# Optimization experiments

Measured on AMD Instinct MI355X. Metric: run time of the kernel, lower is better.

The kernel has to match this reference:

```python
import jax, jax.numpy as jnp
import numpy as np

N_NODES = 50000
N_EDGES = 800000
D = 128          # node/edge feature dim
H = 128          # MLP hidden dim
T_EDGE = 3       # number of edge types
T_NODE = 2       # number of node types


def setup_inputs() -> dict:
    key = jax.random.key(0)
    ks = jax.random.split(key, 14)
    s = 0.05  # weight init scale
    return {
        "nf": jax.random.normal(ks[0], (N_NODES, D), jnp.float32),
        "ef": jax.random.normal(ks[1], (N_EDGES, D), jnp.float32),
        "src": jax.random.randint(ks[2], (N_EDGES,), 0, N_NODES, jnp.int32),
        "dst": jax.random.randint(ks[3], (N_EDGES,), 0, N_NODES, jnp.int32),
        "etype": jax.random.randint(ks[4], (N_EDGES,), 0, T_EDGE, jnp.int32),
        "ntype": jax.random.randint(ks[5], (N_NODES,), 0, T_NODE, jnp.int32),
        # per-edge-type MLP: Linear(3D->H), ReLU, Linear(H->D)
        "We_h": jax.random.normal(ks[6], (T_EDGE, 3 * D, H), jnp.float32) * s,
        "be_h": jnp.zeros((T_EDGE, H), jnp.float32),
        "We_o": jax.random.normal(ks[7], (T_EDGE, H, D), jnp.float32) * s,
        "be_o": jnp.zeros((T_EDGE, D), jnp.float32),
        # per-node-type MLP: Linear(2D->H), ReLU, Linear(H->D)
        "Wn_h": jax.random.normal(ks[8], (T_NODE, 2 * D, H), jnp.float32) * s,
        "bn_h": jnp.zeros((T_NODE, H), jnp.float32),
        "Wn_o": jax.random.normal(ks[9], (T_NODE, H, D), jnp.float32) * s,
        "bn_o": jnp.zeros((T_NODE, D), jnp.float32),
    }


def _typed_mlp(x, tvec, Wh, bh, Wo, bo):
    """Per-type 2-layer MLP dispatch, then the source's gather-back.

    The torch code builds type_pos_list (stable concat of per-type index lists,
    i.e. a stable argsort of tvec) and then indexes the concatenated per-type
    outputs with that same permutation (`updated[type_perm]`, a gather rather
    than an inverse-permutation scatter). We reproduce that exactly:
    out_final[j] = out_correct[perm[perm[j]]].
    """
    T = Wh.shape[0]
    out = jnp.zeros((x.shape[0], Wo.shape[-1]), x.dtype)
    for k in range(T):  # small fixed number of types
        y = jax.nn.relu(x @ Wh[k] + bh[k]) @ Wo[k] + bo[k]
        out = jnp.where((tvec == k)[:, None], y, out)
    perm = jnp.argsort(tvec)  # jax argsort is stable
    return out[perm[perm]]


def reference(nf, ef, src, dst, etype, ntype,
              We_h, be_h, We_o, be_o, Wn_h, bn_h, Wn_o, bn_o):
    # edge update: cat([ef, src_nf, dst_nf]) -> per-type MLP
    em_in = jnp.concatenate([ef, nf[src], nf[dst]], axis=-1)  # [E, 3D]
    new_ef = _typed_mlp(em_in, etype, We_h, be_h, We_o, be_o)  # [E, D]
    # message passing: copy_e('h') messages, sum reduce into dst nodes
    agg_m = jax.ops.segment_sum(new_ef, dst, num_segments=nf.shape[0])  # [N, D]
    # node update: cat([agg_m, nf]) -> per-type MLP
    nm_in = jnp.concatenate([agg_m, nf], axis=-1)  # [N, 2D]
    new_nf = _typed_mlp(nm_in, ntype, Wn_h, bn_h, Wn_o, bn_o)  # [N, D]
    return new_nf, new_ef
```

## Files before the change

### kernel.cpp

```cpp
#include <hip/hip_runtime.h>

typedef __bf16 bf16_t;
typedef bf16_t bf16x8_t __attribute__((ext_vector_type(8)));
typedef float  f32x4_t  __attribute__((ext_vector_type(4)));

#define RCHUNK 4096

__global__ void pack_w_kernel(const float* __restrict__ W, bf16_t* __restrict__ out,
                              int T, int Ksrc, int k0, int KB)
{
  int total = T * KB * 8 * 512;
  for (int idx = blockIdx.x * blockDim.x + threadIdx.x; idx < total;
       idx += gridDim.x * blockDim.x) {
    int j  = idx & 7;
    int l  = (idx >> 3) & 63;
    int nb = (idx >> 9) & 7;
    int r  = idx >> 12;
    int kb = r % KB;
    int t  = r / KB;
    int k = k0 + kb * 32 + ((l >> 4) << 3) + j;
    int n = nb * 16 + (l & 15);
    out[idx] = (bf16_t)W[((size_t)t * Ksrc + k) * 128 + n];
  }
}

template <int T>
__global__ void count_types_kernel(const int* __restrict__ tv, int n,
                                   int* __restrict__ blkcnt)
{
  __shared__ int cnt[T];
  int tid = threadIdx.x, b = blockIdx.x;
  if (tid < T) cnt[tid] = 0;
  __syncthreads();
  int lo = b * RCHUNK, hi = min(n, lo + RCHUNK);
  int loc[T];
#pragma unroll
  for (int t = 0; t < T; ++t) loc[t] = 0;
  for (int i = lo + tid; i < hi; i += 256) {
    int tq = tv[i];
#pragma unroll
    for (int t = 0; t < T; ++t) loc[t] += (tq == t);
  }
#pragma unroll
  for (int t = 0; t < T; ++t)
    if (loc[t]) atomicAdd(&cnt[t], loc[t]);
  __syncthreads();
  if (tid < T) blkcnt[b * T + tid] = cnt[tid];
}

template <int T>
__global__ void scan_blocks_kernel(const int* __restrict__ blkcnt, int nblocks,
                                   int* __restrict__ blkbase)
{
  __shared__ int sh[256];
  __shared__ int tot[T];
  int tid = threadIdx.x;
  int myc[T], excl[T];
#pragma unroll
  for (int t = 0; t < T; ++t) myc[t] = (tid < nblocks) ? blkcnt[tid * T + t] : 0;
#pragma unroll
  for (int t = 0; t < T; ++t) {
    sh[tid] = myc[t];
    __syncthreads();
    for (int off = 1; off < 256; off <<= 1) {
      int v = (tid >= off) ? sh[tid - off] : 0;
      __syncthreads();
      sh[tid] += v;
      __syncthreads();
    }
    excl[t] = sh[tid] - myc[t];
    if (tid == 255) tot[t] = sh[255];
    __syncthreads();
  }
  if (tid < nblocks) {
    int run = 0;
#pragma unroll
    for (int t = 0; t < T; ++t) {
      blkbase[tid * T + t] = run + excl[t];
      run += tot[t];
    }
  }
}

template <int T>
__global__ void write_ranks_kernel(const int* __restrict__ tv, int n,
                                   const int* __restrict__ blkbase,
                                   int* __restrict__ rank, int* __restrict__ perm)
{
  __shared__ int sh[256];
  int tid = threadIdx.x, b = blockIdx.x;
  int lo = b * RCHUNK + tid * 16;
  int tvq[16];
  int myc[T];
#pragma unroll
  for (int t = 0; t < T; ++t) myc[t] = 0;
#pragma unroll
  for (int q = 0; q < 16; ++q) {
    int i = lo + q;
    int tq = (i < n) ? tv[i] : -1;
    tvq[q] = tq;
#pragma unroll
    for (int t = 0; t < T; ++t) myc[t] += (tq == t);
  }
  int mybase[T];
#pragma unroll
  for (int t = 0; t < T; ++t) {
    sh[tid] = myc[t];
    __syncthreads();
    for (int off = 1; off < 256; off <<= 1) {
      int v = (tid >= off) ? sh[tid - off] : 0;
      __syncthreads();
      sh[tid] += v;
      __syncthreads();
    }
    mybase[t] = blkbase[b * T + t] + sh[tid] - myc[t];
    __syncthreads();
  }
#pragma unroll
  for (int q = 0; q < 16; ++q) {
    int tq = tvq[q];
    if (tq < 0) continue;
    int r = 0;
#pragma unroll
    for (int t = 0; t < T; ++t)
      if (tq == t) { r = mybase[t]; mybase[t] = r + 1; }
    rank[lo + q] = r;
    perm[r] = lo + q;
  }
}

__global__ void hist_dst_kernel(const int* __restrict__ dst, int E,
                                int* __restrict__ hist)
{
  int i = blockIdx.x * blockDim.x + threadIdx.x;
  if (i < E) atomicAdd(&hist[dst[i]], 1);
}

__global__ __launch_bounds__(1024) void scan_offsets_kernel(
    const int* __restrict__ hist, int n, int* __restrict__ offsets,
    int* __restrict__ cursor)
{
  __shared__ int sh[1024];
  int tid = threadIdx.x;
  int per = (n + 1023) >> 10;
  int lo = tid * per;
  int s = 0;
  for (int q = 0; q < per; ++q) {
    int i = lo + q;
    if (i < n) s += hist[i];
  }
  sh[tid] = s;
  __syncthreads();
  for (int off = 1; off < 1024; off <<= 1) {
    int v = (tid >= off) ? sh[tid - off] : 0;
    __syncthreads();
    sh[tid] += v;
    __syncthreads();
  }
  int run = sh[tid] - s;
  for (int q = 0; q < per; ++q) {
    int i = lo + q;
    if (i < n) {
      offsets[i] = run;
      cursor[i] = run;
      run += hist[i];
    }
  }
  if (tid == 1023) offsets[n] = sh[1023];
}

__global__ void scatter_dst_kernel(const int* __restrict__ dst, int E,
                                   int* __restrict__ cursor,
                                   int* __restrict__ edge_by_dst)
{
  int i = blockIdx.x * blockDim.x + threadIdx.x;
  if (i < E) {
    int pos = atomicAdd(&cursor[dst[i]], 1);
    edge_by_dst[pos] = i;
  }
}

__global__ __launch_bounds__(256) void aggregate_kernel(
    const float* __restrict__ ef_new, const int* __restrict__ edge_by_dst,
    const int* __restrict__ offsets, float* __restrict__ agg, int Nn)
{
  int gwid = (blockIdx.x * 256 + threadIdx.x) >> 6;
  int l = threadIdx.x & 63;
  int nw = (gridDim.x * 256) >> 6;
  for (int n = gwid; n < Nn; n += nw) {
    int lo = offsets[n], hi = offsets[n + 1];
    float sx = 0.f, sy = 0.f;
    int q = lo;
    for (; q + 1 < hi; q += 2) {
      int e0 = edge_by_dst[q], e1 = edge_by_dst[q + 1];
      float2 v0 = *(const float2*)(ef_new + (size_t)e0 * 128 + l * 2);
      float2 v1 = *(const float2*)(ef_new + (size_t)e1 * 128 + l * 2);
      sx += v0.x + v1.x;
      sy += v0.y + v1.y;
    }
    if (q < hi) {
      int e0 = edge_by_dst[q];
      float2 v0 = *(const float2*)(ef_new + (size_t)e0 * 128 + l * 2);
      sx += v0.x;
      sy += v0.y;
    }
    float2 o;
    o.x = sx; o.y = sy;
    *(float2*)(agg + (size_t)n * 128 + l * 2) = o;
  }
}

__global__ __launch_bounds__(256) void precompute_p_kernel(
    const float* __restrict__ nf,
    const bf16_t* __restrict__ pW1s, const bf16_t* __restrict__ pW1d,
    const bf16_t* __restrict__ pWn1b,
    bf16_t* __restrict__ Ps, bf16_t* __restrict__ Pd, bf16_t* __restrict__ Pn,
    int Nn)
{
  __shared__ char Wsm[32768];
  const int which = blockIdx.x & 7, tile = blockIdx.x >> 3;
  const bf16_t* pB; bf16_t* po;
  if (which < 3)      { pB = pW1s + which * 16384;        po = Ps + (size_t)which * Nn * 128; }
  else if (which < 6) { pB = pW1d + (which - 3) * 16384;  po = Pd + (size_t)(which - 3) * Nn * 128; }
  else                { pB = pWn1b + (which - 6) * 16384; po = Pn + (size_t)(which - 6) * Nn * 128; }

  const int tid = threadIdx.x, l = tid & 63, w = tid >> 6;
  const int rb = (w >> 1) * 32, cb = (w & 1) * 64, l15 = l & 15;
  const int koff = (l >> 4) << 3;

  {
    const uint4* g = (const uint4*)pB;
    uint4* d = (uint4*)Wsm;
#pragma unroll
    for (int q = 0; q < 8; ++q) d[q * 256 + tid] = g[q * 256 + tid];
  }

  const int base = tile * 64;
  const int r0 = base + rb + l15, r1 = r0 + 16;
  const float* q0 = nf + (size_t)min(r0, Nn - 1) * 128 + koff;
  const float* q1 = nf + (size_t)min(r1, Nn - 1) * 128 + koff;
  f32x4_t areg[2][4][2];
#pragma unroll
  for (int kb = 0; kb < 4; ++kb) {
    areg[0][kb][0] = ((const f32x4_t*)(q0 + kb * 32))[0];
    areg[0][kb][1] = ((const f32x4_t*)(q0 + kb * 32))[1];
    areg[1][kb][0] = ((const f32x4_t*)(q1 + kb * 32))[0];
    areg[1][kb][1] = ((const f32x4_t*)(q1 + kb * 32))[1];
  }
  __syncthreads();

  f32x4_t acc[2][4];
#pragma unroll
  for (int m = 0; m < 2; ++m)
#pragma unroll
    for (int n = 0; n < 4; ++n) acc[m][n] = (f32x4_t){0.f, 0.f, 0.f, 0.f};

#pragma unroll
  for (int kb = 0; kb < 4; ++kb) {
    bf16x8_t bfr[4];
#pragma unroll
    for (int n = 0; n < 4; ++n)
      bfr[n] = *(const bf16x8_t*)(Wsm + ((kb * 8 + (cb >> 4) + n) * 64 + l) * 16);
    bf16x8_t a0, a1;
#pragma unroll
    for (int z = 0; z < 4; ++z) {
      a0[z] = (bf16_t)areg[0][kb][0][z]; a0[4 + z] = (bf16_t)areg[0][kb][1][z];
      a1[z] = (bf16_t)areg[1][kb][0][z]; a1[4 + z] = (bf16_t)areg[1][kb][1][z];
    }
#pragma unroll
    for (int n = 0; n < 4; ++n) {
      acc[0][n] = __builtin_amdgcn_mfma_f32_16x16x32_bf16(a0, bfr[n], acc[0][n], 0, 0, 0);
      acc[1][n] = __builtin_amdgcn_mfma_f32_16x16x32_bf16(a1, bfr[n], acc[1][n], 0, 0, 0);
    }
  }

#pragma unroll
  for (int n = 0; n < 4; ++n) {
    int col = cb + 16 * n + l15;
#pragma unroll
    for (int m = 0; m < 2; ++m)
#pragma unroll
      for (int jj = 0; jj < 4; ++jj) {
        int row = rb + 16 * m + ((l >> 4) << 2) + jj;
        int node = base + row;
        if (node < Nn) po[(size_t)node * 128 + col] = (bf16_t)acc[m][n][jj];
      }
  }
}

template <int T, bool EDGE>
__global__ __launch_bounds__(256, 2) void mlp4_kernel(
    const float* __restrict__ feat,
    const int* __restrict__ src, const int* __restrict__ dst,
    const int* __restrict__ perm, const int* __restrict__ rank,
    const int* __restrict__ tbase,
    const bf16_t* __restrict__ pW1, const float* __restrict__ b1,
    const bf16_t* __restrict__ pW2, const float* __restrict__ b2,
    const bf16_t* __restrict__ P1, const bf16_t* __restrict__ P2, int pnodes,
    float* __restrict__ out, int Ntot)
{
  __shared__ char Wsm[32768];
  __shared__ char Psm[16384];
  __shared__ char Hsm[16384];
  __shared__ int sm_e[64], sm_j[64], sm_s0[64], sm_s1[64];

  const int tid = threadIdx.x;
  const int l = tid & 63, w = tid >> 6;
  const int rb = (w >> 1) * 32, cb = (w & 1) * 64;
  const int l15 = l & 15;
  const int koff = (l >> 4) << 3;

  const int s0 = tbase[0];
  const int s1 = (T > 1) ? tbase[1] : Ntot;
  const int s2 = (T > 2) ? tbase[2] : Ntot;
  const int e0t = (T > 1) ? s1 : Ntot;
  const int e1t = (T > 2) ? s2 : Ntot;
  const int c0 = (e0t - s0 + 63) >> 6;
  const int c1 = (T > 1) ? ((e1t - s1 + 63) >> 6) : 0;
  const int c2 = (T > 2) ? ((Ntot - s2 + 63) >> 6) : 0;
  const int cum1 = c0, cum2 = c0 + c1, total = cum2 + c2;

  const int tpb = (total + gridDim.x - 1) / gridDim.x;
  const int pt0 = blockIdx.x * tpb;
  const int pt1 = min(total, pt0 + tpb);

  int cur_t = -1;
  bf16x8_t w2r[16];
  float bh[4], bo[4];

  for (int pt = pt0; pt < pt1; ++pt) {
    const int t = (pt < cum1) ? 0 : ((pt < cum2) ? 1 : 2);
    const int tstart = (t == 0) ? s0 : ((t == 1) ? s1 : s2);
    const int tend = (t == 0) ? e0t : ((t == 1) ? e1t : Ntot);
    const int i = pt - ((t == 0) ? 0 : ((t == 1) ? cum1 : cum2));
    const int pbase = tstart + (i << 6);

    __syncthreads();
    if (tid < 64) {
      int pos = pbase + tid;
      if (pos < tend) {
        int e = perm[pos];
        sm_e[tid] = e;
        sm_j[tid] = rank[pos];
        if (EDGE) { sm_s0[tid] = src[e]; sm_s1[tid] = dst[e]; }
      } else {
        sm_e[tid] = 0; sm_j[tid] = -1;
        if (EDGE) { sm_s0[tid] = 0; sm_s1[tid] = 0; }
      }
    }
    __syncthreads();

    const int ar0 = rb + l15, ar1 = ar0 + 16;
    const float* q0 = feat + (size_t)sm_e[ar0] * 128 + koff;
    const float* q1 = feat + (size_t)sm_e[ar1] * 128 + koff;
    f32x4_t areg[2][4][2];
#pragma unroll
    for (int kb = 0; kb < 4; ++kb) {
      areg[0][kb][0] = ((const f32x4_t*)(q0 + kb * 32))[0];
      areg[0][kb][1] = ((const f32x4_t*)(q0 + kb * 32))[1];
      areg[1][kb][0] = ((const f32x4_t*)(q1 + kb * 32))[0];
      areg[1][kb][1] = ((const f32x4_t*)(q1 + kb * 32))[1];
    }

#pragma unroll
    for (int q = 0; q < 4; ++q) {
      int idx = tid * 4 + q;
      int row = idx >> 4, c8 = idx & 15;
      bf16x8_t s;
      if (EDGE) {
        bf16x8_t u = ((const bf16x8_t*)(P1 + ((size_t)t * pnodes + sm_s0[row]) * 128))[c8];
        bf16x8_t v = ((const bf16x8_t*)(P2 + ((size_t)t * pnodes + sm_s1[row]) * 128))[c8];
#pragma unroll
        for (int z = 0; z < 8; ++z) s[z] = (bf16_t)((float)u[z] + (float)v[z]);
      } else {
        s = ((const bf16x8_t*)(P1 + ((size_t)t * pnodes + sm_e[row]) * 128))[c8];
      }
      *(bf16x8_t*)(Psm + row * 256 + ((c8 ^ (row & 15)) << 4)) = s;
    }

    if (t != cur_t) {
      __syncthreads();
      {
        const uint4* g = (const uint4*)(pW1 + (size_t)t * 16384);
        uint4* d = (uint4*)Wsm;
#pragma unroll
        for (int q = 0; q < 8; ++q) d[q * 256 + tid] = g[q * 256 + tid];
      }
      {
        const bf16x8_t* g2 = (const bf16x8_t*)pW2;
#pragma unroll
        for (int kb = 0; kb < 4; ++kb)
#pragma unroll
          for (int n = 0; n < 4; ++n)
            w2r[kb * 4 + n] = g2[(size_t)((t * 4 + kb) * 8 + (cb >> 4) + n) * 64 + l];
      }
#pragma unroll
      for (int n = 0; n < 4; ++n) {
        bh[n] = b1[t * 128 + cb + 16 * n + l15];
        bo[n] = b2[t * 128 + cb + 16 * n + l15];
      }
      cur_t = t;
      __syncthreads();
    }

    f32x4_t acc[2][4];
#pragma unroll
    for (int m = 0; m < 2; ++m)
#pragma unroll
      for (int n = 0; n < 4; ++n) acc[m][n] = (f32x4_t){0.f, 0.f, 0.f, 0.f};

#pragma unroll
    for (int kb = 0; kb < 4; ++kb) {
      bf16x8_t bfr[4];
#pragma unroll
      for (int n = 0; n < 4; ++n)
        bfr[n] = *(const bf16x8_t*)(Wsm + ((kb * 8 + (cb >> 4) + n) * 64 + l) * 16);
      bf16x8_t a0, a1;
#pragma unroll
      for (int z = 0; z < 4; ++z) {
        a0[z] = (bf16_t)areg[0][kb][0][z]; a0[4 + z] = (bf16_t)areg[0][kb][1][z];
        a1[z] = (bf16_t)areg[1][kb][0][z]; a1[4 + z] = (bf16_t)areg[1][kb][1][z];
      }
#pragma unroll
      for (int n = 0; n < 4; ++n) {
        acc[0][n] = __builtin_amdgcn_mfma_f32_16x16x32_bf16(a0, bfr[n], acc[0][n], 0, 0, 0);
        acc[1][n] = __builtin_amdgcn_mfma_f32_16x16x32_bf16(a1, bfr[n], acc[1][n], 0, 0, 0);
      }
    }

    __syncthreads();
#pragma unroll
    for (int n = 0; n < 4; ++n) {
      int col = cb + 16 * n + l15;
      int byte = col * 2;
#pragma unroll
      for (int m = 0; m < 2; ++m)
#pragma unroll
        for (int jj = 0; jj < 4; ++jj) {
          int row = rb + 16 * m + ((l >> 4) << 2) + jj;
          float pv = (float)*(const bf16_t*)(
              Psm + row * 256 + ((byte & 15) | ((((byte >> 4) ^ (row & 15)) & 15) << 4)));
          float v = acc[m][n][jj] + pv + bh[n];
          v = v > 0.f ? v : 0.f;
          *(bf16_t*)(Hsm + row * 256 + (byte ^ ((row & 7) << 4))) = (bf16_t)v;
        }
    }
    __syncthreads();

    f32x4_t acc2[2][4];
#pragma unroll
    for (int m = 0; m < 2; ++m)
#pragma unroll
      for (int n = 0; n < 4; ++n) acc2[m][n] = (f32x4_t){0.f, 0.f, 0.f, 0.f};

#pragma unroll
    for (int kb = 0; kb < 4; ++kb) {
      int kbyte = kb * 64 + ((l >> 4) << 4);
      int row0 = rb + l15, row1 = row0 + 16;
      bf16x8_t h0 = *(const bf16x8_t*)(Hsm + row0 * 256 + (kbyte ^ ((row0 & 7) << 4)));
      bf16x8_t h1 = *(const bf16x8_t*)(Hsm + row1 * 256 + (kbyte ^ ((row1 & 7) << 4)));
#pragma unroll
      for (int n = 0; n < 4; ++n) {
        acc2[0][n] = __builtin_amdgcn_mfma_f32_16x16x32_bf16(h0, w2r[kb * 4 + n], acc2[0][n], 0, 0, 0);
        acc2[1][n] = __builtin_amdgcn_mfma_f32_16x16x32_bf16(h1, w2r[kb * 4 + n], acc2[1][n], 0, 0, 0);
      }
    }

#pragma unroll
    for (int n = 0; n < 4; ++n) {
      int col = cb + 16 * n + l15;
#pragma unroll
      for (int m = 0; m < 2; ++m)
#pragma unroll
        for (int jj = 0; jj < 4; ++jj) {
          int row = rb + 16 * m + ((l >> 4) << 2) + jj;
          int j = sm_j[row];
          if (j >= 0) out[(size_t)j * 128 + col] = acc2[m][n][jj] + bo[n];
        }
    }
  }
}

extern "C" void kernel_launch(void* const* d_in, const int* in_sizes, int n_in,
                              void* d_out, int out_size, void* d_ws, size_t ws_size,
                              hipStream_t stream)
{
  const float* nf    = (const float*)d_in[0];
  const float* ef    = (const float*)d_in[1];
  const int*   src   = (const int*)d_in[2];
  const int*   dst   = (const int*)d_in[3];
  const int*   etype = (const int*)d_in[4];
  const int*   ntype = (const int*)d_in[5];
  const float* Weh   = (const float*)d_in[6];
  const float* beh   = (const float*)d_in[7];
  const float* Weo   = (const float*)d_in[8];
  const float* beo   = (const float*)d_in[9];
  const float* Wnh   = (const float*)d_in[10];
  const float* bnh   = (const float*)d_in[11];
  const float* Wno   = (const float*)d_in[12];
  const float* bno   = (const float*)d_in[13];

  const int E = in_sizes[2];
  const int N = in_sizes[5];
  const int TE = 3, TN = 2;

  char* ws = (char*)d_ws;
  size_t off = 0;
  auto alloc = [&](size_t bytes) -> char* {
    char* p = ws + off;
    off = (off + bytes + 511) & ~(size_t)511;
    return p;
  };
  bf16_t* pW1e  = (bf16_t*)alloc((size_t)TE * 16384 * 2);
  bf16_t* pW1s  = (bf16_t*)alloc((size_t)TE * 16384 * 2);
  bf16_t* pW1d  = (bf16_t*)alloc((size_t)TE * 16384 * 2);
  bf16_t* pWe2  = (bf16_t*)alloc((size_t)TE * 16384 * 2);
  bf16_t* pWn1a = (bf16_t*)alloc((size_t)TN * 16384 * 2);
  bf16_t* pWn1b = (bf16_t*)alloc((size_t)TN * 16384 * 2);
  bf16_t* pWn2  = (bf16_t*)alloc((size_t)TN * 16384 * 2);
  bf16_t* Ps = (bf16_t*)alloc((size_t)TE * N * 128 * 2);
  bf16_t* Pd = (bf16_t*)alloc((size_t)TE * N * 128 * 2);
  bf16_t* Pn = (bf16_t*)alloc((size_t)TN * N * 128 * 2);
  int* rank_e = (int*)alloc((size_t)E * 4);
  int* perm_e = (int*)alloc((size_t)E * 4);
  int* rank_n = (int*)alloc((size_t)N * 4);
  int* perm_n = (int*)alloc((size_t)N * 4);
  const int NBE = (E + RCHUNK - 1) / RCHUNK;
  const int NBN = (N + RCHUNK - 1) / RCHUNK;
  int* blkcnt_e  = (int*)alloc((size_t)NBE * TE * 4);
  int* blkbase_e = (int*)alloc((size_t)NBE * TE * 4);
  int* blkcnt_n  = (int*)alloc((size_t)NBN * TN * 4);
  int* blkbase_n = (int*)alloc((size_t)NBN * TN * 4);
  float* agg = (float*)alloc((size_t)N * 128 * 4);
  int* dsthist     = (int*)alloc((size_t)N * 4);
  int* dstoffs     = (int*)alloc((size_t)(N + 1) * 4);
  int* dstcursor   = (int*)alloc((size_t)N * 4);
  int* edge_by_dst = (int*)alloc((size_t)E * 4);
  (void)ws_size; (void)n_in; (void)out_size;

  pack_w_kernel<<<192, 256, 0, stream>>>(Weh, pW1e, TE, 384, 0, 4);
  pack_w_kernel<<<192, 256, 0, stream>>>(Weh, pW1s, TE, 384, 128, 4);
  pack_w_kernel<<<192, 256, 0, stream>>>(Weh, pW1d, TE, 384, 256, 4);
  pack_w_kernel<<<192, 256, 0, stream>>>(Weo, pWe2, TE, 128, 0, 4);
  pack_w_kernel<<<128, 256, 0, stream>>>(Wnh, pWn1a, TN, 256, 0, 4);
  pack_w_kernel<<<128, 256, 0, stream>>>(Wnh, pWn1b, TN, 256, 128, 4);
  pack_w_kernel<<<128, 256, 0, stream>>>(Wno, pWn2, TN, 128, 0, 4);

  const int ptiles = (N + 63) / 64;
  precompute_p_kernel<<<ptiles * 8, 256, 0, stream>>>(
      nf, pW1s, pW1d, pWn1b, Ps, Pd, Pn, N);

  count_types_kernel<3><<<NBE, 256, 0, stream>>>(etype, E, blkcnt_e);
  scan_blocks_kernel<3><<<1, 256, 0, stream>>>(blkcnt_e, NBE, blkbase_e);
  write_ranks_kernel<3><<<NBE, 256, 0, stream>>>(etype, E, blkbase_e, rank_e, perm_e);

  count_types_kernel<2><<<NBN, 256, 0, stream>>>(ntype, N, blkcnt_n);
  scan_blocks_kernel<2><<<1, 256, 0, stream>>>(blkcnt_n, NBN, blkbase_n);
  write_ranks_kernel<2><<<NBN, 256, 0, stream>>>(ntype, N, blkbase_n, rank_n, perm_n);

  hipMemsetAsync(dsthist, 0, (size_t)N * 4, stream);
  hist_dst_kernel<<<(E + 255) / 256, 256, 0, stream>>>(dst, E, dsthist);
  scan_offsets_kernel<<<1, 1024, 0, stream>>>(dsthist, N, dstoffs, dstcursor);
  scatter_dst_kernel<<<(E + 255) / 256, 256, 0, stream>>>(dst, E, dstcursor, edge_by_dst);

  float* out_nf = (float*)d_out;
  float* out_ef = (float*)d_out + (size_t)N * 128;

  mlp4_kernel<3, true><<<512, 256, 0, stream>>>(
      ef, src, dst, perm_e, rank_e, blkbase_e,
      pW1e, beh, pWe2, beo, Ps, Pd, N, out_ef, E);

  aggregate_kernel<<<3200, 256, 0, stream>>>(out_ef, edge_by_dst, dstoffs, agg, N);

  mlp4_kernel<2, false><<<512, 256, 0, stream>>>(
      agg, nullptr, nullptr, perm_n, rank_n, blkbase_n,
      pWn1a, bnh, pWn2, bno, Pn, nullptr, N, out_nf, N);
}
```

Baseline: 840.2 us.

## Software-pipeline MLP gathers and aggregate from dst-sorted bf16 slot buffer

The MLP kernel now prefetches the next tile's feature rows and projected P rows while the current tile computes. Per-row metadata comes from precomputed int4 arrays shuffled across lanes, replacing the LDS staging that needed extra barriers. The edge MLP also writes a bf16 copy of each output row into a dst-sorted slot buffer, so aggregation becomes a contiguous streaming read with no indirect fp32 gathers. The precompute kernel uses a persistent grid that loops over tiles. In exchange this adds two metadata kernels, an extra bf16 write stream of the edge outputs, and bf16 rounding in the aggregated sums, which loses some precision.

```diff
diff --git a/kernel.cpp b/kernel.cpp
--- a/kernel.cpp
+++ b/kernel.cpp
@@ -1,10 +1,12 @@
 #include <hip/hip_runtime.h>
 
 typedef __bf16 bf16_t;
+typedef bf16_t bf16x2_t __attribute__((ext_vector_type(2)));
 typedef bf16_t bf16x8_t __attribute__((ext_vector_type(8)));
 typedef float  f32x4_t  __attribute__((ext_vector_type(4)));
 
 #define RCHUNK 4096
+#define MFMA16(a, b, c) __builtin_amdgcn_mfma_f32_16x16x32_bf16((a), (b), (c), 0, 0, 0)
 
 __global__ void pack_w_kernel(const float* __restrict__ W, bf16_t* __restrict__ out,
                               int T, int Ksrc, int k0, int KB)
@@ -171,41 +173,66 @@
 
 __global__ void scatter_dst_kernel(const int* __restrict__ dst, int E,
                                    int* __restrict__ cursor,
-                                   int* __restrict__ edge_by_dst)
+                                   int* __restrict__ dstpos)
+{
+  int i = blockIdx.x * blockDim.x + threadIdx.x;
+  if (i < E) dstpos[i] = atomicAdd(&cursor[dst[i]], 1);
+}
+
+__global__ void gather_meta_edge_kernel(const int* __restrict__ perm,
+                                        const int* __restrict__ rank,
+                                        const int* __restrict__ src,
+                                        const int* __restrict__ dst,
+                                        const int* __restrict__ dstpos,
+                                        int4* __restrict__ meta4,
+                                        int* __restrict__ slotv, int E)
 {
   int i = blockIdx.x * blockDim.x + threadIdx.x;
   if (i < E) {
-    int pos = atomicAdd(&cursor[dst[i]], 1);
-    edge_by_dst[pos] = i;
-  }
-}
-
-__global__ __launch_bounds__(256) void aggregate_kernel(
-    const float* __restrict__ ef_new, const int* __restrict__ edge_by_dst,
-    const int* __restrict__ offsets, float* __restrict__ agg, int Nn)
-{
-  int gwid = (blockIdx.x * 256 + threadIdx.x) >> 6;
+    int e = perm[i], j = rank[i];
+    int4 m;
+    m.x = e; m.y = src[e]; m.z = dst[e]; m.w = j;
+    meta4[i] = m;
+    slotv[i] = dstpos[j];
+  }
+}
+
+__global__ void gather_meta_node_kernel(const int* __restrict__ perm,
+                                        const int* __restrict__ rank,
+                                        int4* __restrict__ meta4, int N)
+{
+  int i = blockIdx.x * blockDim.x + threadIdx.x;
+  if (i < N) {
+    int e = perm[i];
+    int4 m;
+    m.x = e; m.y = e; m.z = e; m.w = rank[i];
+    meta4[i] = m;
+  }
+}
+
+__global__ __launch_bounds__(256) void aggregate_slots_kernel(
+    const bf16_t* __restrict__ slot_buf, const int* __restrict__ offsets,
+    float* __restrict__ agg, int Nn)
+{
+  int gw = (blockIdx.x * 256 + threadIdx.x) >> 6;
   int l = threadIdx.x & 63;
   int nw = (gridDim.x * 256) >> 6;
-  for (int n = gwid; n < Nn; n += nw) {
+  for (int n = gw; n < Nn; n += nw) {
     int lo = offsets[n], hi = offsets[n + 1];
     float sx = 0.f, sy = 0.f;
     int q = lo;
     for (; q + 1 < hi; q += 2) {
-      int e0 = edge_by_dst[q], e1 = edge_by_dst[q + 1];
-      float2 v0 = *(const float2*)(ef_new + (size_t)e0 * 128 + l * 2);
-      float2 v1 = *(const float2*)(ef_new + (size_t)e1 * 128 + l * 2);
-      sx += v0.x + v1.x;
-      sy += v0.y + v1.y;
+      bf16x2_t v0 = *(const bf16x2_t*)(slot_buf + (size_t)q * 128 + l * 2);
+      bf16x2_t v1 = *(const bf16x2_t*)(slot_buf + (size_t)(q + 1) * 128 + l * 2);
+      sx += (float)v0[0] + (float)v1[0];
+      sy += (float)v0[1] + (float)v1[1];
     }
     if (q < hi) {
-      int e0 = edge_by_dst[q];
-      float2 v0 = *(const float2*)(ef_new + (size_t)e0 * 128 + l * 2);
-      sx += v0.x;
-      sy += v0.y;
-    }
-    float2 o;
-    o.x = sx; o.y = sy;
+      bf16x2_t v0 = *(const bf16x2_t*)(slot_buf + (size_t)q * 128 + l * 2);
+      sx += (float)v0[0];
+      sy += (float)v0[1];
+    }
+    float2 o; o.x = sx; o.y = sy;
     *(float2*)(agg + (size_t)n * 128 + l * 2) = o;
   }
 }
@@ -215,10 +242,11 @@
     const bf16_t* __restrict__ pW1s, const bf16_t* __restrict__ pW1d,
     const bf16_t* __restrict__ pWn1b,
     bf16_t* __restrict__ Ps, bf16_t* __restrict__ Pd, bf16_t* __restrict__ Pn,
-    int Nn)
+    int Nn, int nseg)
 {
   __shared__ char Wsm[32768];
-  const int which = blockIdx.x & 7, tile = blockIdx.x >> 3;
+  const int which = blockIdx.x & 7;
+  const int seg = blockIdx.x >> 3;
   const bf16_t* pB; bf16_t* po;
   if (which < 3)      { pB = pW1s + which * 16384;        po = Ps + (size_t)which * Nn * 128; }
   else if (which < 6) { pB = pW1d + (which - 3) * 16384;  po = Pd + (size_t)(which - 3) * Nn * 128; }
@@ -234,75 +262,73 @@
 #pragma unroll
     for (int q = 0; q < 8; ++q) d[q * 256 + tid] = g[q * 256 + tid];
   }
-
-  const int base = tile * 64;
-  const int r0 = base + rb + l15, r1 = r0 + 16;
-  const float* q0 = nf + (size_t)min(r0, Nn - 1) * 128 + koff;
-  const float* q1 = nf + (size_t)min(r1, Nn - 1) * 128 + koff;
-  f32x4_t areg[2][4][2];
-#pragma unroll
-  for (int kb = 0; kb < 4; ++kb) {
-    areg[0][kb][0] = ((const f32x4_t*)(q0 + kb * 32))[0];
-    areg[0][kb][1] = ((const f32x4_t*)(q0 + kb * 32))[1];
-    areg[1][kb][0] = ((const f32x4_t*)(q1 + kb * 32))[0];
-    areg[1][kb][1] = ((const f32x4_t*)(q1 + kb * 32))[1];
-  }
   __syncthreads();
 
-  f32x4_t acc[2][4];
-#pragma unroll
-  for (int m = 0; m < 2; ++m)
-#pragma unroll
-    for (int n = 0; n < 4; ++n) acc[m][n] = (f32x4_t){0.f, 0.f, 0.f, 0.f};
-
-#pragma unroll
-  for (int kb = 0; kb < 4; ++kb) {
-    bf16x8_t bfr[4];
-#pragma unroll
-    for (int n = 0; n < 4; ++n)
-      bfr[n] = *(const bf16x8_t*)(Wsm + ((kb * 8 + (cb >> 4) + n) * 64 + l) * 16);
-    bf16x8_t a0, a1;
-#pragma unroll
-    for (int z = 0; z < 4; ++z) {
-      a0[z] = (bf16_t)areg[0][kb][0][z]; a0[4 + z] = (bf16_t)areg[0][kb][1][z];
-      a1[z] = (bf16_t)areg[1][kb][0][z]; a1[4 + z] = (bf16_t)areg[1][kb][1][z];
+  const int ntiles = (Nn + 63) >> 6;
+  for (int tile = seg; tile < ntiles; tile += nseg) {
+    const int base = tile * 64;
+    const int r0 = min(base + rb + l15, Nn - 1);
+    const int r1 = min(base + rb + l15 + 16, Nn - 1);
+    const float* q0 = nf + (size_t)r0 * 128 + koff;
+    const float* q1 = nf + (size_t)r1 * 128 + koff;
+    f32x4_t areg[16];
+#pragma unroll
+    for (int kb = 0; kb < 4; ++kb) {
+      areg[kb * 2]     = ((const f32x4_t*)(q0 + kb * 32))[0];
+      areg[kb * 2 + 1] = ((const f32x4_t*)(q0 + kb * 32))[1];
+      areg[8 + kb * 2]     = ((const f32x4_t*)(q1 + kb * 32))[0];
+      areg[8 + kb * 2 + 1] = ((const f32x4_t*)(q1 + kb * 32))[1];
+    }
+    f32x4_t acc[2][4];
+#pragma unroll
+    for (int m = 0; m < 2; ++m)
+#pragma unroll
+      for (int n = 0; n < 4; ++n) acc[m][n] = (f32x4_t){0.f, 0.f, 0.f, 0.f};
+#pragma unroll
+    for (int kb = 0; kb < 4; ++kb) {
+      bf16x8_t bfr[4];
+#pragma unroll
+      for (int n = 0; n < 4; ++n)
+        bfr[n] = *(const bf16x8_t*)(Wsm + ((kb * 8 + (cb >> 4) + n) * 64 + l) * 16);
+      bf16x8_t a0, a1;
+#pragma unroll
+      for (int z = 0; z < 4; ++z) {
+        a0[z] = (bf16_t)areg[kb * 2][z];     a0[4 + z] = (bf16_t)areg[kb * 2 + 1][z];
+        a1[z] = (bf16_t)areg[8 + kb * 2][z]; a1[4 + z] = (bf16_t)areg[8 + kb * 2 + 1][z];
+      }
+#pragma unroll
+      for (int n = 0; n < 4; ++n) {
+        acc[0][n] = MFMA16(a0, bfr[n], acc[0][n]);
+        acc[1][n] = MFMA16(a1, bfr[n], acc[1][n]);
+      }
     }
 #pragma unroll
     for (int n = 0; n < 4; ++n) {
-      acc[0][n] = __builtin_amdgcn_mfma_f32_16x16x32_bf16(a0, bfr[n], acc[0][n], 0, 0, 0);
-      acc[1][n] = __builtin_amdgcn_mfma_f32_16x16x32_bf16(a1, bfr[n], acc[1][n], 0, 0, 0);
-    }
-  }
-
-#pragma unroll
-  for (int n = 0; n < 4; ++n) {
-    int col = cb + 16 * n + l15;
-#pragma unroll
-    for (int m = 0; m < 2; ++m)
-#pragma unroll
-      for (int jj = 0; jj < 4; ++jj) {
-        int row = rb + 16 * m + ((l >> 4) << 2) + jj;
-        int node = base + row;
-        if (node < Nn) po[(size_t)node * 128 + col] = (bf16_t)acc[m][n][jj];
-      }
+      int col = cb + 16 * n + l15;
+#pragma unroll
+      for (int m = 0; m < 2; ++m)
+#pragma unroll
+        for (int jj = 0; jj < 4; ++jj) {
+          int row = rb + 16 * m + ((l >> 4) << 2) + jj;
+          int node = base + row;
+          if (node < Nn) po[(size_t)node * 128 + col] = (bf16_t)acc[m][n][jj];
+        }
+    }
   }
 }
 
 template <int T, bool EDGE>
-__global__ __launch_bounds__(256, 2) void mlp4_kernel(
+__global__ __launch_bounds__(256, 2) void mlp5_kernel(
     const float* __restrict__ feat,
-    const int* __restrict__ src, const int* __restrict__ dst,
-    const int* __restrict__ perm, const int* __restrict__ rank,
+    const int4* __restrict__ meta4, const int* __restrict__ slotv,
     const int* __restrict__ tbase,
     const bf16_t* __restrict__ pW1, const float* __restrict__ b1,
     const bf16_t* __restrict__ pW2, const float* __restrict__ b2,
     const bf16_t* __restrict__ P1, const bf16_t* __restrict__ P2, int pnodes,
-    float* __restrict__ out, int Ntot)
+    float* __restrict__ out, bf16_t* __restrict__ slot_out, int Ntot)
 {
   __shared__ char Wsm[32768];
-  __shared__ char Psm[16384];
   __shared__ char Hsm[16384];
-  __shared__ int sm_e[64], sm_j[64], sm_s0[64], sm_s1[64];
 
   const int tid = threadIdx.x;
   const int l = tid & 63, w = tid >> 6;
@@ -323,62 +349,78 @@
   const int tpb = (total + gridDim.x - 1) / gridDim.x;
   const int pt0 = blockIdx.x * tpb;
   const int pt1 = min(total, pt0 + tpb);
-
-  int cur_t = -1;
+  if (pt0 >= pt1) return;
+
+  auto tinfo_t = [&](int pt) -> int {
+    return (pt < cum1) ? 0 : ((pt < cum2) ? 1 : 2);
+  };
+  auto tinfo_base = [&](int pt) -> int {
+    return (pt < cum1) ? s0 + (pt << 6)
+         : (pt < cum2) ? s1 + ((pt - cum1) << 6)
+                       : s2 + ((pt - cum2) << 6);
+  };
+  auto tinfo_end = [&](int pt) -> int {
+    return (pt < cum1) ? e0t : ((pt < cum2) ? e1t : Ntot);
+  };
+  auto load_meta = [&](int pt, int4& m, int& sl) {
+    int pos = tinfo_base(pt) + l;
+    int p = min(pos, Ntot - 1);
+    m = meta4[p];
+    if (EDGE) sl = slotv[p];
+    if (pos >= tinfo_end(pt)) m.w = -1;
+  };
+
+  const int prow = (w << 4) + (l >> 2);
+  const int pcb  = (l & 3) << 2;
+
+  int4 m_cur, m_nxt;
+  int sl_cur = 0, sl_nxt = 0;
+  f32x4_t Af[16];
+  bf16x8_t uP[4], vP[4], ps[4];
   bf16x8_t w2r[16];
   float bh[4], bo[4];
+  int t_cur = -1;
+
+  load_meta(pt0, m_cur, sl_cur);
+  {
+    int e0 = __shfl(m_cur.x, rb + l15);
+    int e1 = __shfl(m_cur.x, rb + l15 + 16);
+    const float* q0 = feat + (size_t)e0 * 128 + koff;
+    const float* q1 = feat + (size_t)e1 * 128 + koff;
+#pragma unroll
+    for (int kb = 0; kb < 4; ++kb) {
+      Af[kb * 2]     = ((const f32x4_t*)(q0 + kb * 32))[0];
+      Af[kb * 2 + 1] = ((const f32x4_t*)(q0 + kb * 32))[1];
+      Af[8 + kb * 2]     = ((const f32x4_t*)(q1 + kb * 32))[0];
+      Af[8 + kb * 2 + 1] = ((const f32x4_t*)(q1 + kb * 32))[1];
+    }
+    int t0 = tinfo_t(pt0);
+    int a = __shfl(EDGE ? m_cur.y : m_cur.x, prow);
+    const bf16x8_t* pu = (const bf16x8_t*)(P1 + ((size_t)t0 * pnodes + a) * 128);
+#pragma unroll
+    for (int q = 0; q < 4; ++q) uP[q] = pu[pcb + q];
+    if (EDGE) {
+      int bi = __shfl(m_cur.z, prow);
+      const bf16x8_t* pv = (const bf16x8_t*)(P2 + ((size_t)t0 * pnodes + bi) * 128);
+#pragma unroll
+      for (int q = 0; q < 4; ++q) vP[q] = pv[pcb + q];
+    }
+  }
+  if (EDGE) {
+#pragma unroll
+    for (int q = 0; q < 4; ++q)
+#pragma unroll
+      for (int z = 0; z < 8; ++z)
+        ps[q][z] = (bf16_t)((float)uP[q][z] + (float)vP[q][z]);
+  } else {
+#pragma unroll
+    for (int q = 0; q < 4; ++q) ps[q] = uP[q];
+  }
+  load_meta(min(pt0 + 1, pt1 - 1), m_nxt, sl_nxt);
 
   for (int pt = pt0; pt < pt1; ++pt) {
-    const int t = (pt < cum1) ? 0 : ((pt < cum2) ? 1 : 2);
-    const int tstart = (t == 0) ? s0 : ((t == 1) ? s1 : s2);
-    const int tend = (t == 0) ? e0t : ((t == 1) ? e1t : Ntot);
-    const int i = pt - ((t == 0) ? 0 : ((t == 1) ? cum1 : cum2));
-    const int pbase = tstart + (i << 6);
-
-    __syncthreads();
-    if (tid < 64) {
-      int pos = pbase + tid;
-      if (pos < tend) {
-        int e = perm[pos];
-        sm_e[tid] = e;
-        sm_j[tid] = rank[pos];
-        if (EDGE) { sm_s0[tid] = src[e]; sm_s1[tid] = dst[e]; }
-      } else {
-        sm_e[tid] = 0; sm_j[tid] = -1;
-        if (EDGE) { sm_s0[tid] = 0; sm_s1[tid] = 0; }
-      }
-    }
-    __syncthreads();
-
-    const int ar0 = rb + l15, ar1 = ar0 + 16;
-    const float* q0 = feat + (size_t)sm_e[ar0] * 128 + koff;
-    const float* q1 = feat + (size_t)sm_e[ar1] * 128 + koff;
-    f32x4_t areg[2][4][2];
-#pragma unroll
-    for (int kb = 0; kb < 4; ++kb) {
-      areg[0][kb][0] = ((const f32x4_t*)(q0 + kb * 32))[0];
-      areg[0][kb][1] = ((const f32x4_t*)(q0 + kb * 32))[1];
-      areg[1][kb][0] = ((const f32x4_t*)(q1 + kb * 32))[0];
-      areg[1][kb][1] = ((const f32x4_t*)(q1 + kb * 32))[1];
-    }
-
-#pragma unroll
-    for (int q = 0; q < 4; ++q) {
-      int idx = tid * 4 + q;
-      int row = idx >> 4, c8 = idx & 15;
-      bf16x8_t s;
-      if (EDGE) {
-        bf16x8_t u = ((const bf16x8_t*)(P1 + ((size_t)t * pnodes + sm_s0[row]) * 128))[c8];
-        bf16x8_t v = ((const bf16x8_t*)(P2 + ((size_t)t * pnodes + sm_s1[row]) * 128))[c8];
-#pragma unroll
-        for (int z = 0; z < 8; ++z) s[z] = (bf16_t)((float)u[z] + (float)v[z]);
-      } else {
-        s = ((const bf16x8_t*)(P1 + ((size_t)t * pnodes + sm_e[row]) * 128))[c8];
-      }
-      *(bf16x8_t*)(Psm + row * 256 + ((c8 ^ (row & 15)) << 4)) = s;
-    }
-
-    if (t != cur_t) {
+    const int t = tinfo_t(pt);
+    if (t != t_cur) {
       __syncthreads();
       {
         const uint4* g = (const uint4*)(pW1 + (size_t)t * 16384);
@@ -399,7 +441,7 @@
         bh[n] = b1[t * 128 + cb + 16 * n + l15];
         bo[n] = b2[t * 128 + cb + 16 * n + l15];
       }
-      cur_t = t;
+      t_cur = t;
       __syncthreads();
     }
 
@@ -408,27 +450,74 @@
     for (int m = 0; m < 2; ++m)
 #pragma unroll
       for (int n = 0; n < 4; ++n) acc[m][n] = (f32x4_t){0.f, 0.f, 0.f, 0.f};
-
+    bf16x8_t a0[4], a1[4];
+#pragma unroll
+    for (int kb = 0; kb < 4; ++kb)
+#pragma unroll
+      for (int z = 0; z < 4; ++z) {
+        a0[kb][z]     = (bf16_t)Af[kb * 2][z];
+        a0[kb][4 + z] = (bf16_t)Af[kb * 2 + 1][z];
+        a1[kb][z]     = (bf16_t)Af[8 + kb * 2][z];
+        a1[kb][4 + z] = (bf16_t)Af[8 + kb * 2 + 1][z];
+      }
 #pragma unroll
     for (int kb = 0; kb < 4; ++kb) {
       bf16x8_t bfr[4];
 #pragma unroll
       for (int n = 0; n < 4; ++n)
         bfr[n] = *(const bf16x8_t*)(Wsm + ((kb * 8 + (cb >> 4) + n) * 64 + l) * 16);
-      bf16x8_t a0, a1;
-#pragma unroll
-      for (int z = 0; z < 4; ++z) {
-        a0[z] = (bf16_t)areg[0][kb][0][z]; a0[4 + z] = (bf16_t)areg[0][kb][1][z];
-        a1[z] = (bf16_t)areg[1][kb][0][z]; a1[4 + z] = (bf16_t)areg[1][kb][1][z];
-      }
 #pragma unroll
       for (int n = 0; n < 4; ++n) {
-        acc[0][n] = __builtin_amdgcn_mfma_f32_16x16x32_bf16(a0, bfr[n], acc[0][n], 0, 0, 0);
-        acc[1][n] = __builtin_amdgcn_mfma_f32_16x16x32_bf16(a1, bfr[n], acc[1][n], 0, 0, 0);
-      }
-    }
-
-    __syncthreads();
+        acc[0][n] = MFMA16(a0[kb], bfr[n], acc[0][n]);
+        acc[1][n] = MFMA16(a1[kb], bfr[n], acc[1][n]);
+      }
+    }
+
+    const int ptn = min(pt + 1, pt1 - 1);
+    {
+      int e0 = __shfl(m_nxt.x, rb + l15);
+      int e1 = __shfl(m_nxt.x, rb + l15 + 16);
+      const float* q0 = feat + (size_t)e0 * 128 + koff;
+      const float* q1 = feat + (size_t)e1 * 128 + koff;
+#pragma unroll
+      for (int kb = 0; kb < 4; ++kb) {
+        Af[kb * 2]     = ((const f32x4_t*)(q0 + kb * 32))[0];
+        Af[kb * 2 + 1] = ((const f32x4_t*)(q0 + kb * 32))[1];
+        Af[8 + kb * 2]     = ((const f32x4_t*)(q1 + kb * 32))[0];
+        Af[8 + kb * 2 + 1] = ((const f32x4_t*)(q1 + kb * 32))[1];
+      }
+    }
+
+    __syncthreads();
+
+    {
+      char* base = Hsm + prow * 256;
+#pragma unroll
+      for (int q = 0; q < 4; ++q)
+        *(bf16x8_t*)(base + ((((pcb + q) << 4)) ^ ((prow & 7) << 4))) = ps[q];
+    }
+
+    {
+      int tn = tinfo_t(ptn);
+      int a = __shfl(EDGE ? m_nxt.y : m_nxt.x, prow);
+      const bf16x8_t* pu = (const bf16x8_t*)(P1 + ((size_t)tn * pnodes + a) * 128);
+#pragma unroll
+      for (int q = 0; q < 4; ++q) uP[q] = pu[pcb + q];
+      if (EDGE) {
+        int bi = __shfl(m_nxt.z, prow);
+        const bf16x8_t* pv = (const bf16x8_t*)(P2 + ((size_t)tn * pnodes + bi) * 128);
+#pragma unroll
+        for (int q = 0; q < 4; ++q) vP[q] = pv[pcb + q];
+      }
+    }
+
+    const int4 m_use = m_cur;
+    const int sl_use = sl_cur;
+    m_cur = m_nxt; sl_cur = sl_nxt;
+    load_meta(min(pt + 2, pt1 - 1), m_nxt, sl_nxt);
+
+    __syncthreads();
+
 #pragma unroll
     for (int n = 0; n < 4; ++n) {
       int col = cb + 16 * n + l15;
@@ -438,13 +527,14 @@
 #pragma unroll
         for (int jj = 0; jj < 4; ++jj) {
           int row = rb + 16 * m + ((l >> 4) << 2) + jj;
-          float pv = (float)*(const bf16_t*)(
-              Psm + row * 256 + ((byte & 15) | ((((byte >> 4) ^ (row & 15)) & 15) << 4)));
+          char* addr = Hsm + row * 256 + (byte ^ ((row & 7) << 4));
+          float pv = (float)*(const bf16_t*)addr;
           float v = acc[m][n][jj] + pv + bh[n];
           v = v > 0.f ? v : 0.f;
-          *(bf16_t*)(Hsm + row * 256 + (byte ^ ((row & 7) << 4))) = (bf16_t)v;
+          *(bf16_t*)addr = (bf16_t)v;
         }
     }
+
     __syncthreads();
 
     f32x4_t acc2[2][4];
@@ -452,7 +542,6 @@
     for (int m = 0; m < 2; ++m)
 #pragma unroll
       for (int n = 0; n < 4; ++n) acc2[m][n] = (f32x4_t){0.f, 0.f, 0.f, 0.f};
-
 #pragma unroll
     for (int kb = 0; kb < 4; ++kb) {
       int kbyte = kb * 64 + ((l >> 4) << 4);
@@ -461,11 +550,20 @@
       bf16x8_t h1 = *(const bf16x8_t*)(Hsm + row1 * 256 + (kbyte ^ ((row1 & 7) << 4)));
 #pragma unroll
       for (int n = 0; n < 4; ++n) {
-        acc2[0][n] = __builtin_amdgcn_mfma_f32_16x16x32_bf16(h0, w2r[kb * 4 + n], acc2[0][n], 0, 0, 0);
-        acc2[1][n] = __builtin_amdgcn_mfma_f32_16x16x32_bf16(h1, w2r[kb * 4 + n], acc2[1][n], 0, 0, 0);
-      }
-    }
-
+        acc2[0][n] = MFMA16(h0, w2r[kb * 4 + n], acc2[0][n]);
+        acc2[1][n] = MFMA16(h1, w2r[kb * 4 + n], acc2[1][n]);
+      }
+    }
+
+    int jrow[2][4], srow[2][4];
+#pragma unroll
+    for (int m = 0; m < 2; ++m)
+#pragma unroll
+      for (int jj = 0; jj < 4; ++jj) {
+        int row = rb + 16 * m + ((l >> 4) << 2) + jj;
+        jrow[m][jj] = __shfl(m_use.w, row);
+        srow[m][jj] = EDGE ? __shfl(sl_use, row) : 0;
+      }
 #pragma unroll
     for (int n = 0; n < 4; ++n) {
       int col = cb + 16 * n + l15;
@@ -473,10 +571,24 @@
       for (int m = 0; m < 2; ++m)
 #pragma unroll
         for (int jj = 0; jj < 4; ++jj) {
-          int row = rb + 16 * m + ((l >> 4) << 2) + jj;
-          int j = sm_j[row];
-          if (j >= 0) out[(size_t)j * 128 + col] = acc2[m][n][jj] + bo[n];
+          int j = jrow[m][jj];
+          if (j >= 0) {
+            float v = acc2[m][n][jj] + bo[n];
+            out[(size_t)j * 128 + col] = v;
+            if (EDGE) slot_out[(size_t)srow[m][jj] * 128 + col] = (bf16_t)v;
+          }
         }
+    }
+
+    if (EDGE) {
+#pragma unroll
+      for (int q = 0; q < 4; ++q)
+#pragma unroll
+        for (int z = 0; z < 8; ++z)
+          ps[q][z] = (bf16_t)((float)uP[q][z] + (float)vP[q][z]);
+    } else {
+#pragma unroll
+      for (int q = 0; q < 4; ++q) ps[q] = uP[q];
     }
   }
 }
@@ -532,10 +644,14 @@
   int* blkcnt_n  = (int*)alloc((size_t)NBN * TN * 4);
   int* blkbase_n = (int*)alloc((size_t)NBN * TN * 4);
   float* agg = (float*)alloc((size_t)N * 128 * 4);
-  int* dsthist     = (int*)alloc((size_t)N * 4);
-  int* dstoffs     = (int*)alloc((size_t)(N + 1) * 4);
-  int* dstcursor   = (int*)alloc((size_t)N * 4);
-  int* edge_by_dst = (int*)alloc((size_t)E * 4);
+  int* dsthist   = (int*)alloc((size_t)N * 4);
+  int* dstoffs   = (int*)alloc((size_t)(N + 1) * 4);
+  int* dstcursor = (int*)alloc((size_t)N * 4);
+  int* dstpos    = (int*)alloc((size_t)E * 4);
+  int4* meta4_e  = (int4*)alloc((size_t)E * 16);
+  int*  slotv_e  = (int*)alloc((size_t)E * 4);
+  int4* meta4_n  = (int4*)alloc((size_t)N * 16);
+  bf16_t* slot_buf = (bf16_t*)alloc((size_t)E * 128 * 2);
   (void)ws_size; (void)n_in; (void)out_size;
 
   pack_w_kernel<<<192, 256, 0, stream>>>(Weh, pW1e, TE, 384, 0, 4);
@@ -546,9 +662,8 @@
   pack_w_kernel<<<128, 256, 0, stream>>>(Wnh, pWn1b, TN, 256, 128, 4);
   pack_w_kernel<<<128, 256, 0, stream>>>(Wno, pWn2, TN, 128, 0, 4);
 
-  const int ptiles = (N + 63) / 64;
-  precompute_p_kernel<<<ptiles * 8, 256, 0, stream>>>(
-      nf, pW1s, pW1d, pWn1b, Ps, Pd, Pn, N);
+  precompute_p_kernel<<<8 * 128, 256, 0, stream>>>(
+      nf, pW1s, pW1d, pWn1b, Ps, Pd, Pn, N, 128);
 
   count_types_kernel<3><<<NBE, 256, 0, stream>>>(etype, E, blkcnt_e);
   scan_blocks_kernel<3><<<1, 256, 0, stream>>>(blkcnt_e, NBE, blkbase_e);
@@ -561,18 +676,23 @@
   hipMemsetAsync(dsthist, 0, (size_t)N * 4, stream);
   hist_dst_kernel<<<(E + 255) / 256, 256, 0, stream>>>(dst, E, dsthist);
   scan_offsets_kernel<<<1, 1024, 0, stream>>>(dsthist, N, dstoffs, dstcursor);
-  scatter_dst_kernel<<<(E + 255) / 256, 256, 0, stream>>>(dst, E, dstcursor, edge_by_dst);
+  scatter_dst_kernel<<<(E + 255) / 256, 256, 0, stream>>>(dst, E, dstcursor, dstpos);
+
+  gather_meta_edge_kernel<<<(E + 255) / 256, 256, 0, stream>>>(
+      perm_e, rank_e, src, dst, dstpos, meta4_e, slotv_e, E);
+  gather_meta_node_kernel<<<(N + 255) / 256, 256, 0, stream>>>(
+      perm_n, rank_n, meta4_n, N);
 
   float* out_nf = (float*)d_out;
   float* out_ef = (float*)d_out + (size_t)N * 128;
 
-  mlp4_kernel<3, true><<<512, 256, 0, stream>>>(
-      ef, src, dst, perm_e, rank_e, blkbase_e,
-      pW1e, beh, pWe2, beo, Ps, Pd, N, out_ef, E);
-
-  aggregate_kernel<<<3200, 256, 0, stream>>>(out_ef, edge_by_dst, dstoffs, agg, N);
-
-  mlp4_kernel<2, false><<<512, 256, 0, stream>>>(
-      agg, nullptr, nullptr, perm_n, rank_n, blkbase_n,
-      pWn1a, bnh, pWn2, bno, Pn, nullptr, N, out_nf, N);
-}
+  mlp5_kernel<3, true><<<512, 256, 0, stream>>>(
+      ef, meta4_e, slotv_e, blkbase_e,
+      pW1e, beh, pWe2, beo, Ps, Pd, N, out_ef, slot_buf, E);
+
+  aggregate_slots_kernel<<<3200, 256, 0, stream>>>(slot_buf, dstoffs, agg, N);
+
+  mlp5_kernel<2, false><<<512, 256, 0, stream>>>(
+      agg, meta4_n, nullptr, blkbase_n,
+      pWn1a, bnh, pWn2, bno, Pn, nullptr, N, out_nf, nullptr, N);
+}
```

Result: slower. 1.020 ms (+21.3%).
